# Performance work log

Hardware: AMD Instinct MI355X
Metric: run time of the kernel (lower is better)

## Reference

```python
import jax, jax.numpy as jnp
import numpy as np

N_NODES = 100000
N_EDGES = 1600000
NFEAT, NHID, NCLASS = 128, 64, 40


def setup_inputs() -> dict:
    key = jax.random.key(0)
    k = jax.random.split(key, 6)
    x = jax.random.normal(k[0], (N_NODES, NFEAT), dtype=jnp.float32)
    edge_index = jax.random.randint(k[1], (2, N_EDGES), 0, N_NODES, dtype=jnp.int64)
    edge_weight = jax.random.uniform(k[2], (N_EDGES,), dtype=jnp.float32)
    # Glorot-style init as in PyG GCNConv.reset_parameters
    W1 = jax.random.normal(k[3], (NFEAT, NHID), dtype=jnp.float32) * (1.0 / np.sqrt(NFEAT))
    b1 = jnp.zeros((NHID,), dtype=jnp.float32)
    W2 = jax.random.normal(k[4], (NHID, NCLASS), dtype=jnp.float32) * (1.0 / np.sqrt(NHID))
    b2 = jnp.zeros((NCLASS,), dtype=jnp.float32)
    return {"x": x, "edge_index": edge_index, "edge_weight": edge_weight,
            "W1": W1, "b1": b1, "W2": W2, "b2": b2}


def _gcn_conv(x, edge_index, edge_weight, W, b):
    """PyG GCNConv: add self-loops, symmetric gcn_norm, linear, scatter-add, bias."""
    n = x.shape[0]
    loop = jnp.arange(n)
    row = jnp.concatenate([edge_index[0], loop])  # source nodes
    col = jnp.concatenate([edge_index[1], loop])  # target nodes
    w = jnp.concatenate([edge_weight, jnp.ones((n,), edge_weight.dtype)])
    deg = jax.ops.segment_sum(w, col, num_segments=n)          # [N]
    dinv = jnp.where(deg > 0, jax.lax.rsqrt(deg), 0.0)
    norm = dinv[row] * w * dinv[col]                           # [E+N]
    h = x @ W                                                  # [N, out]
    msg = norm[:, None] * h[row]                               # gather: [E+N, out]
    out = jax.ops.segment_sum(msg, col, num_segments=n)        # scatter-add: [N, out]
    return out + b


def reference(x, edge_index, edge_weight, W1, b1, W2, b2):
    h = jax.nn.relu(_gcn_conv(x, edge_index, edge_weight, W1, b1))
    # F.dropout with training=False is identity (eval mode)
    return _gcn_conv(h, edge_index, edge_weight, W2, b2)
```

## Files before the change

kernel.cpp:

```cpp
#include <hip/hip_runtime.h>
#include <hip/hip_bf16.h>

#define N_NODES 100000
#define N_EDGES 1600000
#define NFEAT 128
#define NHID 64
#define NCLASS 40
#define CAP 64

#define BIN_SHIFT 9
#define BIN_NODES 512
#define NBIN ((N_NODES + BIN_NODES - 1) / BIN_NODES)
#define SCAP 10240
#define CHUNK 2048
#define LCAP 16

using frag_ab = __attribute__((ext_vector_type(8))) short;
using frag_cd = __attribute__((ext_vector_type(4))) float;


__device__ __forceinline__ unsigned pack2(float a, float b) {
    unsigned ua = __float_as_uint(a), ub = __float_as_uint(b);
    unsigned ra = (ua + 0x7FFFu + ((ua >> 16) & 1u)) >> 16;
    unsigned rb = (ub + 0x7FFFu + ((ub >> 16) & 1u)) >> 16;
    return ra | (rb << 16);
}
__device__ __forceinline__ unsigned short bf16rtn(float f) {
    unsigned u = __float_as_uint(f);
    return (unsigned short)((u + 0x7FFFu + ((u >> 16) & 1u)) >> 16);
}
__device__ __forceinline__ float lo16(unsigned w) { return __uint_as_float(w << 16); }
__device__ __forceinline__ float hi16(unsigned w) { return __uint_as_float(w & 0xFFFF0000u); }


__global__ __launch_bounds__(256) void bin_kernel(const int* __restrict__ ei,
                                                  const float* __restrict__ ew,
                                                  int* __restrict__ bincnt,
                                                  uint2* __restrict__ staging) {
    __shared__ int lcnt[NBIN];
    __shared__ int gbase[NBIN];
    __shared__ int scanbuf[256];
    __shared__ int totals;
    __shared__ uint2 lbuf[NBIN * LCAP];
    int t = threadIdx.x;
    for (int i = t; i < NBIN; i += 256) lcnt[i] = 0;
    __syncthreads();

    int base = blockIdx.x * CHUNK;
#pragma unroll
    for (int u = 0; u < CHUNK / 256; ++u) {
        int e = base + u * 256 + t;
        if (e < N_EDGES) {
            int c = ei[N_EDGES + e];
            int r = ei[e];
            float w = ew[e];
            unsigned wq = (unsigned)fminf(w * 32768.0f, 32767.0f);
            uint2 en = make_uint2(((unsigned)r << 15) | wq, (unsigned)c);
            int b = c >> BIN_SHIFT;
            int p = atomicAdd(&lcnt[b], 1);
            if (p < LCAP) {
                lbuf[b * LCAP + p] = en;
            } else {
                int g = atomicAdd(&bincnt[b], 1);
                if (g < SCAP) staging[(size_t)b * SCAP + g] = en;
            }
        }
    }
    __syncthreads();

    int clamped = (t < NBIN) ? min(lcnt[t], LCAP) : 0;
    if (t < NBIN) gbase[t] = (clamped > 0) ? atomicAdd(&bincnt[t], clamped) : 0;
    scanbuf[t] = clamped;
    __syncthreads();
    for (int o = 1; o < 256; o <<= 1) {
        int add = (t >= o) ? scanbuf[t - o] : 0;
        __syncthreads();
        scanbuf[t] += add;
        __syncthreads();
    }
    if (t < NBIN) lcnt[t] = scanbuf[t] - clamped;
    if (t == NBIN - 1) totals = scanbuf[t];
    __syncthreads();

    int total = totals;
    for (int i = t; i < total; i += 256) {
        int lo = 0, hi = NBIN - 1;
#pragma unroll
        for (int s = 0; s < 8; ++s) {
            int mid = (lo + hi + 1) >> 1;
            if (lcnt[mid] <= i) lo = mid; else hi = mid - 1;
        }
        int idx = i - lcnt[lo];
        int gp = gbase[lo] + idx;
        if (gp < SCAP) staging[(size_t)lo * SCAP + gp] = lbuf[lo * LCAP + idx];
    }
}


__global__ __launch_bounds__(256) void place_kernel(const int* __restrict__ bincnt,
                                                    const uint2* __restrict__ staging,
                                                    unsigned* __restrict__ bucket,
                                                    int* __restrict__ cnt,
                                                    float* __restrict__ dinv) {
    __shared__ int lpos[BIN_NODES];
    __shared__ float lws[BIN_NODES];
    int b = blockIdx.x;
    int t = threadIdx.x;
    for (int i = t; i < BIN_NODES; i += 256) { lpos[i] = 0; lws[i] = 0.0f; }
    __syncthreads();

    int nodebase = b << BIN_SHIFT;
    int n = bincnt[b];
    if (n > SCAP) n = SCAP;
    const uint2* st = staging + (size_t)b * SCAP;
    for (int i = t; i < n; i += 256) {
        uint2 en = st[i];
        int local = (int)en.y - nodebase;
        int p = atomicAdd(&lpos[local], 1);
        if (p < CAP) bucket[((size_t)en.y << 6) + p] = en.x;
        atomicAdd(&lws[local], (float)(en.x & 32767u) * (1.0f / 32768.0f));
    }
    __syncthreads();
    for (int i = t; i < BIN_NODES; i += 256) {
        int node = nodebase + i;
        if (node < N_NODES) {
            cnt[node] = min(lpos[i], CAP);
            dinv[node] = rsqrtf(1.0f + lws[i]);
        }
    }
}


__global__ __launch_bounds__(256) void w1prep_kernel(const float* __restrict__ W1,
                                                     unsigned short* __restrict__ w1t) {
    int idx = blockIdx.x * 256 + threadIdx.x;
    if (idx < NFEAT * NHID) {
        int k = idx >> 6, n = idx & 63;
        w1t[n * NFEAT + k] = bf16rtn(W1[idx]);
    }
}


__global__ __launch_bounds__(256) void gemm1_kernel(const float* __restrict__ x,
                                                    const unsigned short* __restrict__ w1t,
                                                    unsigned short* __restrict__ h1b) {
    __shared__ unsigned short sm[16384];
    int t = threadIdx.x;
    int row0 = blockIdx.x * 64;

#pragma unroll
    for (int p = 0; p < 4; ++p) {
        int id = p * 256 + t;
        int r = id >> 4;
        int c = id & 15;
        int gr = row0 + r; if (gr > N_NODES - 1) gr = N_NODES - 1;
        const float* src = x + (size_t)gr * NFEAT + c * 8;
        float4 f0 = *(const float4*)src;
        float4 f1 = *(const float4*)(src + 4);
        uint4 pk = make_uint4(pack2(f0.x, f0.y), pack2(f0.z, f0.w),
                              pack2(f1.x, f1.y), pack2(f1.z, f1.w));
        int cs = c ^ (r & 15);
        *(uint4*)(&sm[r * 128 + cs * 8]) = pk;
    }
    const uint4* wt4 = (const uint4*)w1t;
#pragma unroll
    for (int p = 0; p < 4; ++p) {
        int id = p * 256 + t;
        int n = id >> 4;
        int c = id & 15;
        uint4 v = wt4[id];
        int cs = c ^ (n & 15);
        *(uint4*)(&sm[8192 + n * 128 + cs * 8]) = v;
    }
    __syncthreads();

    int w = t >> 6, l = t & 63;
    int li = l & 15, q = l >> 4;
    int arow = w * 16 + li;

    frag_cd acc0 = {0.f, 0.f, 0.f, 0.f};
    frag_cd acc1 = {0.f, 0.f, 0.f, 0.f};
    frag_cd acc2 = {0.f, 0.f, 0.f, 0.f};
    frag_cd acc3 = {0.f, 0.f, 0.f, 0.f};

#pragma unroll
    for (int kc = 0; kc < 4; ++kc) {
        int cc = (kc * 4 + q) ^ li;
        frag_ab a  = *(const frag_ab*)(&sm[arow * 128 + cc * 8]);
        frag_ab b0 = *(const frag_ab*)(&sm[8192 + (0 * 16 + li) * 128 + cc * 8]);
        frag_ab b1 = *(const frag_ab*)(&sm[8192 + (1 * 16 + li) * 128 + cc * 8]);
        frag_ab b2 = *(const frag_ab*)(&sm[8192 + (2 * 16 + li) * 128 + cc * 8]);
        frag_ab b3 = *(const frag_ab*)(&sm[8192 + (3 * 16 + li) * 128 + cc * 8]);
        acc0 = __builtin_amdgcn_mfma_f32_16x16x32_bf16(a, b0, acc0, 0, 0, 0);
        acc1 = __builtin_amdgcn_mfma_f32_16x16x32_bf16(a, b1, acc1, 0, 0, 0);
        acc2 = __builtin_amdgcn_mfma_f32_16x16x32_bf16(a, b2, acc2, 0, 0, 0);
        acc3 = __builtin_amdgcn_mfma_f32_16x16x32_bf16(a, b3, acc3, 0, 0, 0);
    }

#pragma unroll
    for (int reg = 0; reg < 4; ++reg) {
        int rrow = row0 + w * 16 + q * 4 + reg;
        if (rrow < N_NODES) {
            unsigned short* dst = h1b + (size_t)rrow * NHID + li;
            dst[0]  = bf16rtn(acc0[reg]);
            dst[16] = bf16rtn(acc1[reg]);
            dst[32] = bf16rtn(acc2[reg]);
            dst[48] = bf16rtn(acc3[reg]);
        }
    }
}


__global__ __launch_bounds__(256) void gather1_kernel(
        const int* __restrict__ cnt, const unsigned* __restrict__ bucket,
        const float* __restrict__ dinv, const unsigned short* __restrict__ h1b,
        const float* __restrict__ b1, float* __restrict__ relu1) {
    int t = threadIdx.x;
    int lane = t & 63;
    int wave = t >> 6;
    int g = lane >> 3;
    int l = lane & 7;
    int node = (blockIdx.x * 4 + wave) * 8 + g;
    bool nvalid = node < N_NODES;
    int nd = nvalid ? node : N_NODES - 1;
    int d = cnt[nd];
    float dc = dinv[nd];

    uint4 eb0 = *(const uint4*)(bucket + ((size_t)nd << 6) + l * 8);
    uint4 eb1 = *(const uint4*)(bucket + ((size_t)nd << 6) + l * 8 + 4);
    int rl[8]; float wl[8];
#pragma unroll
    for (int k = 0; k < 8; ++k) {
        unsigned e = (k < 4) ? ((const unsigned*)&eb0)[k] : ((const unsigned*)&eb1)[k - 4];
        int slot = l * 8 + k;
        bool ok = slot < d;
        int r = ok ? (int)(e >> 15) : 0;
        rl[k] = r;
        wl[k] = ok ? (float)(e & 32767u) * (1.0f / 32768.0f) * dinv[r] : 0.0f;
    }

    uint4 hs = *(const uint4*)(h1b + (size_t)nd * NHID + l * 8);
    float acc[8];
#pragma unroll
    for (int k = 0; k < 4; ++k) {
        unsigned w = ((const unsigned*)&hs)[k];
        acc[2 * k] = dc * lo16(w);
        acc[2 * k + 1] = dc * hi16(w);
    }

    for (int j = 0; j < d; j += 8) {
        int src = (g << 3) + (j >> 3);
        int r[8]; float w[8];
#pragma unroll
        for (int k = 0; k < 8; ++k) { r[k] = __shfl(rl[k], src); w[k] = __shfl(wl[k], src); }
        uint4 v[8];
#pragma unroll
        for (int k = 0; k < 8; ++k)
            v[k] = *(const uint4*)(h1b + (size_t)r[k] * NHID + l * 8);
#pragma unroll
        for (int k = 0; k < 8; ++k) {
#pragma unroll
            for (int q = 0; q < 4; ++q) {
                unsigned ww = ((const unsigned*)&v[k])[q];
                acc[2 * q] += w[k] * lo16(ww);
                acc[2 * q + 1] += w[k] * hi16(ww);
            }
        }
    }
    if (nvalid) {
        float4 bv0 = *(const float4*)(b1 + l * 8);
        float4 bv1 = *(const float4*)(b1 + l * 8 + 4);
        float4 o0 = make_float4(fmaxf(dc * acc[0] + bv0.x, 0.0f), fmaxf(dc * acc[1] + bv0.y, 0.0f),
                                fmaxf(dc * acc[2] + bv0.z, 0.0f), fmaxf(dc * acc[3] + bv0.w, 0.0f));
        float4 o1 = make_float4(fmaxf(dc * acc[4] + bv1.x, 0.0f), fmaxf(dc * acc[5] + bv1.y, 0.0f),
                                fmaxf(dc * acc[6] + bv1.z, 0.0f), fmaxf(dc * acc[7] + bv1.w, 0.0f));
        *(float4*)(relu1 + (size_t)node * NHID + l * 8) = o0;
        *(float4*)(relu1 + (size_t)node * NHID + l * 8 + 4) = o1;
    }
}


__global__ __launch_bounds__(256) void gemm2_kernel(const float* __restrict__ in,
                                                    const float* __restrict__ W2,
                                                    unsigned short* __restrict__ h2b) {
    __shared__ float sB[NHID * NCLASS];
    int t = threadIdx.x;
    for (int i = t; i < NHID * NCLASS; i += 256) sB[i] = W2[i];
    __syncthreads();

    int row = blockIdx.x * 256 + t;
    bool valid = row < N_NODES;
    int r = valid ? row : N_NODES - 1;
    float acc[NCLASS] = {};

#pragma unroll 2
    for (int k = 0; k < NHID; k += 4) {
        float4 a = *(const float4*)(in + (size_t)r * NHID + k);
#pragma unroll
        for (int kk = 0; kk < 4; ++kk) {
            float av = (kk == 0) ? a.x : (kk == 1) ? a.y : (kk == 2) ? a.z : a.w;
#pragma unroll
            for (int cg = 0; cg < 10; ++cg) {
                float4 bb = *(const float4*)(sB + (k + kk) * NCLASS + cg * 4);
                acc[cg * 4 + 0] += av * bb.x;
                acc[cg * 4 + 1] += av * bb.y;
                acc[cg * 4 + 2] += av * bb.z;
                acc[cg * 4 + 3] += av * bb.w;
            }
        }
    }
    if (valid) {
#pragma unroll
        for (int cg = 0; cg < 5; ++cg) {
            uint4 p;
            p.x = pack2(acc[cg * 8 + 0], acc[cg * 8 + 1]);
            p.y = pack2(acc[cg * 8 + 2], acc[cg * 8 + 3]);
            p.z = pack2(acc[cg * 8 + 4], acc[cg * 8 + 5]);
            p.w = pack2(acc[cg * 8 + 6], acc[cg * 8 + 7]);
            *(uint4*)(h2b + (size_t)row * NCLASS + cg * 8) = p;
        }
    }
}


__global__ __launch_bounds__(256) void gather2_kernel(
        const int* __restrict__ cnt, const unsigned* __restrict__ bucket,
        const float* __restrict__ dinv, const unsigned short* __restrict__ h2b,
        const float* __restrict__ b2, float* __restrict__ out) {
    int t = threadIdx.x;
    int lane = t & 63;
    int wave = t >> 6;
    int g = lane >> 4;
    int l = lane & 15;
    int node = (blockIdx.x * 4 + wave) * 4 + g;
    bool nvalid = node < N_NODES;
    int nd = nvalid ? node : N_NODES - 1;
    int d = cnt[nd];
    float dc = dinv[nd];
    bool fvalid = (l < 10);

    uint4 eb = *(const uint4*)(bucket + ((size_t)nd << 6) + l * 4);
    int rl[4]; float wl[4];
#pragma unroll
    for (int k = 0; k < 4; ++k) {
        unsigned e = ((const unsigned*)&eb)[k];
        int slot = l * 4 + k;
        bool ok = slot < d;
        int r = ok ? (int)(e >> 15) : 0;
        rl[k] = r;
        wl[k] = ok ? (float)(e & 32767u) * (1.0f / 32768.0f) * dinv[r] : 0.0f;
    }

    float acc[4] = {};
    int lc = fvalid ? l * 4 : 0;
    if (fvalid) {
        uint2 hs = *(const uint2*)(h2b + (size_t)nd * NCLASS + lc);
        acc[0] = dc * lo16(hs.x); acc[1] = dc * hi16(hs.x);
        acc[2] = dc * lo16(hs.y); acc[3] = dc * hi16(hs.y);
    }

    for (int j = 0; j < d; j += 4) {
        int src = (g << 4) + (j >> 2);
        int r0 = __shfl(rl[0], src), r1 = __shfl(rl[1], src);
        int r2 = __shfl(rl[2], src), r3 = __shfl(rl[3], src);
        float w0 = __shfl(wl[0], src), w1 = __shfl(wl[1], src);
        float w2 = __shfl(wl[2], src), w3 = __shfl(wl[3], src);
        if (fvalid) {
            uint2 v0 = *(const uint2*)(h2b + (size_t)r0 * NCLASS + lc);
            uint2 v1 = *(const uint2*)(h2b + (size_t)r1 * NCLASS + lc);
            uint2 v2 = *(const uint2*)(h2b + (size_t)r2 * NCLASS + lc);
            uint2 v3 = *(const uint2*)(h2b + (size_t)r3 * NCLASS + lc);
            acc[0] += w0 * lo16(v0.x) + w1 * lo16(v1.x) + w2 * lo16(v2.x) + w3 * lo16(v3.x);
            acc[1] += w0 * hi16(v0.x) + w1 * hi16(v1.x) + w2 * hi16(v2.x) + w3 * hi16(v3.x);
            acc[2] += w0 * lo16(v0.y) + w1 * lo16(v1.y) + w2 * lo16(v2.y) + w3 * lo16(v3.y);
            acc[3] += w0 * hi16(v0.y) + w1 * hi16(v1.y) + w2 * hi16(v2.y) + w3 * hi16(v3.y);
        }
    }
    if (nvalid && fvalid) {
        float4 bv = *(const float4*)(b2 + l * 4);
        *(float4*)(out + (size_t)node * NCLASS + l * 4) =
            make_float4(dc * acc[0] + bv.x, dc * acc[1] + bv.y,
                        dc * acc[2] + bv.z, dc * acc[3] + bv.w);
    }
}


extern "C" void kernel_launch(void* const* d_in, const int* in_sizes, int n_in,
                              void* d_out, int out_size, void* d_ws, size_t ws_size,
                              hipStream_t stream) {
    const float* x  = (const float*)d_in[0];
    const int*   ei = (const int*)d_in[1];
    const float* ew = (const float*)d_in[2];
    const float* W1 = (const float*)d_in[3];
    const float* b1 = (const float*)d_in[4];
    const float* W2 = (const float*)d_in[5];
    const float* b2 = (const float*)d_in[6];
    float* out = (float*)d_out;

    int*            bincnt = (int*)d_ws;
    int*            cnt    = bincnt + 256;
    float*          dinv   = (float*)(cnt + 100352);
    unsigned*       bucket = (unsigned*)(dinv + 100352);
    unsigned short* h1b    = (unsigned short*)(bucket + (size_t)N_NODES * CAP);
    float*          relu1  = (float*)(h1b + (size_t)N_NODES * NHID);
    unsigned short* w1t    = (unsigned short*)(relu1 + (size_t)N_NODES * NHID);
    uint2*          staging = (uint2*)relu1;
    unsigned short* h2b    = h1b;

    hipMemsetAsync(bincnt, 0, NBIN * sizeof(int), stream);

    w1prep_kernel<<<32, 256, 0, stream>>>(W1, w1t);
    bin_kernel<<<(N_EDGES + CHUNK - 1) / CHUNK, 256, 0, stream>>>(ei, ew, bincnt, staging);
    place_kernel<<<NBIN, 256, 0, stream>>>(bincnt, staging, bucket, cnt, dinv);

    gemm1_kernel<<<(N_NODES + 63) / 64, 256, 0, stream>>>(x, w1t, h1b);
    gather1_kernel<<<(N_NODES + 31) / 32, 256, 0, stream>>>(cnt, bucket, dinv, h1b, b1, relu1);

    gemm2_kernel<<<(N_NODES + 255) / 256, 256, 0, stream>>>(relu1, W2, h2b);
    gather2_kernel<<<(N_NODES + 15) / 16, 256, 0, stream>>>(cnt, bucket, dinv, h2b, b2, out);
}
```

Baseline: 275.4 us.

## Use MFMA bf16 for second GEMM, store relu1 as bf16, simplify binning

The second GEMM now runs on bf16 MFMA 16x16x32 instructions. Its operands are staged in swizzled LDS tiles, and W2 is pre-transposed to bf16 in a merged prep kernel. The first aggregation writes its ReLU output as bf16 instead of fp32, which halves that intermediate traffic. Edge binning switches from a local-buffer-plus-scan scheme to a two-pass count/reserve/scatter with smaller chunks, and place_kernel uses 512 threads. The risks are extra bf16 rounding on the hidden activations and one more workgroup barrier pass in binning.

```diff
diff --git a/kernel.cpp b/kernel.cpp
--- a/kernel.cpp
+++ b/kernel.cpp
@@ -12,8 +12,7 @@
 #define BIN_NODES 512
 #define NBIN ((N_NODES + BIN_NODES - 1) / BIN_NODES)
 #define SCAP 10240
-#define CHUNK 2048
-#define LCAP 16
+#define CHUNK 1024
 
 using frag_ab = __attribute__((ext_vector_type(8))) short;
 using frag_cd = __attribute__((ext_vector_type(4))) float;
@@ -39,65 +38,49 @@
                                                   uint2* __restrict__ staging) {
     __shared__ int lcnt[NBIN];
     __shared__ int gbase[NBIN];
-    __shared__ int scanbuf[256];
-    __shared__ int totals;
-    __shared__ uint2 lbuf[NBIN * LCAP];
     int t = threadIdx.x;
     for (int i = t; i < NBIN; i += 256) lcnt[i] = 0;
     __syncthreads();
 
     int base = blockIdx.x * CHUNK;
-#pragma unroll
-    for (int u = 0; u < CHUNK / 256; ++u) {
+    int c[4]; int rr[4]; float w[4];
+#pragma unroll
+    for (int u = 0; u < 4; ++u) {
         int e = base + u * 256 + t;
         if (e < N_EDGES) {
-            int c = ei[N_EDGES + e];
-            int r = ei[e];
-            float w = ew[e];
-            unsigned wq = (unsigned)fminf(w * 32768.0f, 32767.0f);
-            uint2 en = make_uint2(((unsigned)r << 15) | wq, (unsigned)c);
-            int b = c >> BIN_SHIFT;
-            int p = atomicAdd(&lcnt[b], 1);
-            if (p < LCAP) {
-                lbuf[b * LCAP + p] = en;
-            } else {
-                int g = atomicAdd(&bincnt[b], 1);
-                if (g < SCAP) staging[(size_t)b * SCAP + g] = en;
-            }
-        }
-    }
-    __syncthreads();
-
-    int clamped = (t < NBIN) ? min(lcnt[t], LCAP) : 0;
-    if (t < NBIN) gbase[t] = (clamped > 0) ? atomicAdd(&bincnt[t], clamped) : 0;
-    scanbuf[t] = clamped;
-    __syncthreads();
-    for (int o = 1; o < 256; o <<= 1) {
-        int add = (t >= o) ? scanbuf[t - o] : 0;
-        __syncthreads();
-        scanbuf[t] += add;
-        __syncthreads();
-    }
-    if (t < NBIN) lcnt[t] = scanbuf[t] - clamped;
-    if (t == NBIN - 1) totals = scanbuf[t];
-    __syncthreads();
-
-    int total = totals;
-    for (int i = t; i < total; i += 256) {
-        int lo = 0, hi = NBIN - 1;
-#pragma unroll
-        for (int s = 0; s < 8; ++s) {
-            int mid = (lo + hi + 1) >> 1;
-            if (lcnt[mid] <= i) lo = mid; else hi = mid - 1;
-        }
-        int idx = i - lcnt[lo];
-        int gp = gbase[lo] + idx;
-        if (gp < SCAP) staging[(size_t)lo * SCAP + gp] = lbuf[lo * LCAP + idx];
-    }
-}
-
-
-__global__ __launch_bounds__(256) void place_kernel(const int* __restrict__ bincnt,
+            c[u] = ei[N_EDGES + e];
+            rr[u] = ei[e];
+            w[u] = ew[e];
+        } else {
+            c[u] = -1;
+        }
+    }
+#pragma unroll
+    for (int u = 0; u < 4; ++u)
+        if (c[u] >= 0) atomicAdd(&lcnt[c[u] >> BIN_SHIFT], 1);
+    __syncthreads();
+    if (t < NBIN) {
+        int n = lcnt[t];
+        gbase[t] = (n > 0) ? atomicAdd(&bincnt[t], n) : 0;
+    }
+    __syncthreads();
+    if (t < NBIN) lcnt[t] = 0;
+    __syncthreads();
+#pragma unroll
+    for (int u = 0; u < 4; ++u) {
+        if (c[u] >= 0) {
+            int b = c[u] >> BIN_SHIFT;
+            unsigned wq = (unsigned)fminf(w[u] * 32768.0f, 32767.0f);
+            int p = gbase[b] + atomicAdd(&lcnt[b], 1);
+            if (p < SCAP)
+                staging[(size_t)b * SCAP + p] =
+                    make_uint2(((unsigned)rr[u] << 15) | wq, (unsigned)c[u]);
+        }
+    }
+}
+
+
+__global__ __launch_bounds__(512) void place_kernel(const int* __restrict__ bincnt,
                                                     const uint2* __restrict__ staging,
                                                     unsigned* __restrict__ bucket,
                                                     int* __restrict__ cnt,
@@ -106,14 +89,14 @@
     __shared__ float lws[BIN_NODES];
     int b = blockIdx.x;
     int t = threadIdx.x;
-    for (int i = t; i < BIN_NODES; i += 256) { lpos[i] = 0; lws[i] = 0.0f; }
+    for (int i = t; i < BIN_NODES; i += 512) { lpos[i] = 0; lws[i] = 0.0f; }
     __syncthreads();
 
     int nodebase = b << BIN_SHIFT;
     int n = bincnt[b];
     if (n > SCAP) n = SCAP;
     const uint2* st = staging + (size_t)b * SCAP;
-    for (int i = t; i < n; i += 256) {
+    for (int i = t; i < n; i += 512) {
         uint2 en = st[i];
         int local = (int)en.y - nodebase;
         int p = atomicAdd(&lpos[local], 1);
@@ -121,7 +104,7 @@
         atomicAdd(&lws[local], (float)(en.x & 32767u) * (1.0f / 32768.0f));
     }
     __syncthreads();
-    for (int i = t; i < BIN_NODES; i += 256) {
+    for (int i = t; i < BIN_NODES; i += 512) {
         int node = nodebase + i;
         if (node < N_NODES) {
             cnt[node] = min(lpos[i], CAP);
@@ -131,12 +114,19 @@
 }
 
 
-__global__ __launch_bounds__(256) void w1prep_kernel(const float* __restrict__ W1,
-                                                     unsigned short* __restrict__ w1t) {
+__global__ __launch_bounds__(256) void prep_kernel(const float* __restrict__ W1,
+                                                   const float* __restrict__ W2,
+                                                   unsigned short* __restrict__ w1t,
+                                                   unsigned short* __restrict__ w2t) {
     int idx = blockIdx.x * 256 + threadIdx.x;
     if (idx < NFEAT * NHID) {
         int k = idx >> 6, n = idx & 63;
         w1t[n * NFEAT + k] = bf16rtn(W1[idx]);
+    }
+    int idx2 = idx - NFEAT * NHID;
+    if (idx2 >= 0 && idx2 < NHID * NCLASS) {
+        int k = idx2 / NCLASS, n = idx2 - k * NCLASS;
+        w2t[n * NHID + k] = bf16rtn(W2[idx2]);
     }
 }
 
@@ -214,7 +204,7 @@
 __global__ __launch_bounds__(256) void gather1_kernel(
         const int* __restrict__ cnt, const unsigned* __restrict__ bucket,
         const float* __restrict__ dinv, const unsigned short* __restrict__ h1b,
-        const float* __restrict__ b1, float* __restrict__ relu1) {
+        const float* __restrict__ b1, unsigned short* __restrict__ relu1b) {
     int t = threadIdx.x;
     int lane = t & 63;
     int wave = t >> 6;
@@ -270,54 +260,70 @@
     if (nvalid) {
         float4 bv0 = *(const float4*)(b1 + l * 8);
         float4 bv1 = *(const float4*)(b1 + l * 8 + 4);
-        float4 o0 = make_float4(fmaxf(dc * acc[0] + bv0.x, 0.0f), fmaxf(dc * acc[1] + bv0.y, 0.0f),
-                                fmaxf(dc * acc[2] + bv0.z, 0.0f), fmaxf(dc * acc[3] + bv0.w, 0.0f));
-        float4 o1 = make_float4(fmaxf(dc * acc[4] + bv1.x, 0.0f), fmaxf(dc * acc[5] + bv1.y, 0.0f),
-                                fmaxf(dc * acc[6] + bv1.z, 0.0f), fmaxf(dc * acc[7] + bv1.w, 0.0f));
-        *(float4*)(relu1 + (size_t)node * NHID + l * 8) = o0;
-        *(float4*)(relu1 + (size_t)node * NHID + l * 8 + 4) = o1;
-    }
-}
-
-
-__global__ __launch_bounds__(256) void gemm2_kernel(const float* __restrict__ in,
-                                                    const float* __restrict__ W2,
+        float o0 = fmaxf(dc * acc[0] + bv0.x, 0.0f), o1 = fmaxf(dc * acc[1] + bv0.y, 0.0f);
+        float o2 = fmaxf(dc * acc[2] + bv0.z, 0.0f), o3 = fmaxf(dc * acc[3] + bv0.w, 0.0f);
+        float o4 = fmaxf(dc * acc[4] + bv1.x, 0.0f), o5 = fmaxf(dc * acc[5] + bv1.y, 0.0f);
+        float o6 = fmaxf(dc * acc[6] + bv1.z, 0.0f), o7 = fmaxf(dc * acc[7] + bv1.w, 0.0f);
+        uint4 pk = make_uint4(pack2(o0, o1), pack2(o2, o3), pack2(o4, o5), pack2(o6, o7));
+        *(uint4*)(relu1b + (size_t)node * NHID + l * 8) = pk;
+    }
+}
+
+
+__global__ __launch_bounds__(256) void gemm2_kernel(const unsigned short* __restrict__ relu1b,
+                                                    const unsigned short* __restrict__ w2t,
                                                     unsigned short* __restrict__ h2b) {
-    __shared__ float sB[NHID * NCLASS];
-    int t = threadIdx.x;
-    for (int i = t; i < NHID * NCLASS; i += 256) sB[i] = W2[i];
-    __syncthreads();
-
-    int row = blockIdx.x * 256 + t;
-    bool valid = row < N_NODES;
-    int r = valid ? row : N_NODES - 1;
-    float acc[NCLASS] = {};
-
-#pragma unroll 2
-    for (int k = 0; k < NHID; k += 4) {
-        float4 a = *(const float4*)(in + (size_t)r * NHID + k);
-#pragma unroll
-        for (int kk = 0; kk < 4; ++kk) {
-            float av = (kk == 0) ? a.x : (kk == 1) ? a.y : (kk == 2) ? a.z : a.w;
-#pragma unroll
-            for (int cg = 0; cg < 10; ++cg) {
-                float4 bb = *(const float4*)(sB + (k + kk) * NCLASS + cg * 4);
-                acc[cg * 4 + 0] += av * bb.x;
-                acc[cg * 4 + 1] += av * bb.y;
-                acc[cg * 4 + 2] += av * bb.z;
-                acc[cg * 4 + 3] += av * bb.w;
-            }
-        }
-    }
-    if (valid) {
-#pragma unroll
-        for (int cg = 0; cg < 5; ++cg) {
-            uint4 p;
-            p.x = pack2(acc[cg * 8 + 0], acc[cg * 8 + 1]);
-            p.y = pack2(acc[cg * 8 + 2], acc[cg * 8 + 3]);
-            p.z = pack2(acc[cg * 8 + 4], acc[cg * 8 + 5]);
-            p.w = pack2(acc[cg * 8 + 6], acc[cg * 8 + 7]);
-            *(uint4*)(h2b + (size_t)row * NCLASS + cg * 8) = p;
+    __shared__ unsigned short sa[64 * 64];
+    __shared__ unsigned short sb[48 * 64];
+    int t = threadIdx.x;
+    int row0 = blockIdx.x * 64;
+
+#pragma unroll
+    for (int p = 0; p < 2; ++p) {
+        int id = p * 256 + t;
+        int r = id >> 3, cj = id & 7;
+        int gr = row0 + r; if (gr > N_NODES - 1) gr = N_NODES - 1;
+        uint4 v = *(const uint4*)(relu1b + (size_t)gr * NHID + cj * 8);
+        int cs = cj ^ (r & 7);
+        *(uint4*)(&sa[r * 64 + cs * 8]) = v;
+    }
+    for (int id = t; id < 384; id += 256) {
+        int n = id >> 3, cj = id & 7;
+        uint4 v = make_uint4(0u, 0u, 0u, 0u);
+        if (n < NCLASS) v = *(const uint4*)(w2t + n * NHID + cj * 8);
+        int cs = cj ^ (n & 7);
+        *(uint4*)(&sb[n * 64 + cs * 8]) = v;
+    }
+    __syncthreads();
+
+    int w = t >> 6, l = t & 63;
+    int li = l & 15, q = l >> 4;
+    int arow = w * 16 + li;
+
+    frag_cd acc0 = {0.f, 0.f, 0.f, 0.f};
+    frag_cd acc1 = {0.f, 0.f, 0.f, 0.f};
+    frag_cd acc2 = {0.f, 0.f, 0.f, 0.f};
+
+#pragma unroll
+    for (int kc = 0; kc < 2; ++kc) {
+        int cc = (kc * 4 + q) ^ (li & 7);
+        frag_ab a  = *(const frag_ab*)(&sa[arow * 64 + cc * 8]);
+        frag_ab b0 = *(const frag_ab*)(&sb[(0 + li) * 64 + cc * 8]);
+        frag_ab b1 = *(const frag_ab*)(&sb[(16 + li) * 64 + cc * 8]);
+        frag_ab b2 = *(const frag_ab*)(&sb[(32 + li) * 64 + cc * 8]);
+        acc0 = __builtin_amdgcn_mfma_f32_16x16x32_bf16(a, b0, acc0, 0, 0, 0);
+        acc1 = __builtin_amdgcn_mfma_f32_16x16x32_bf16(a, b1, acc1, 0, 0, 0);
+        acc2 = __builtin_amdgcn_mfma_f32_16x16x32_bf16(a, b2, acc2, 0, 0, 0);
+    }
+
+#pragma unroll
+    for (int reg = 0; reg < 4; ++reg) {
+        int rrow = row0 + w * 16 + q * 4 + reg;
+        if (rrow < N_NODES) {
+            unsigned short* dst = h2b + (size_t)rrow * NCLASS;
+            dst[li] = bf16rtn(acc0[reg]);
+            dst[16 + li] = bf16rtn(acc1[reg]);
+            if (li < 8) dst[32 + li] = bf16rtn(acc2[reg]);
         }
     }
 }
@@ -397,25 +403,27 @@
     const float* b2 = (const float*)d_in[6];
     float* out = (float*)d_out;
 
-    int*            bincnt = (int*)d_ws;
-    int*            cnt    = bincnt + 256;
-    float*          dinv   = (float*)(cnt + 100352);
-    unsigned*       bucket = (unsigned*)(dinv + 100352);
-    unsigned short* h1b    = (unsigned short*)(bucket + (size_t)N_NODES * CAP);
-    float*          relu1  = (float*)(h1b + (size_t)N_NODES * NHID);
-    unsigned short* w1t    = (unsigned short*)(relu1 + (size_t)N_NODES * NHID);
-    uint2*          staging = (uint2*)relu1;
-    unsigned short* h2b    = h1b;
+    int*            bincnt  = (int*)d_ws;
+    int*            cnt     = bincnt + 256;
+    float*          dinv    = (float*)(cnt + 100352);
+    unsigned*       bucket  = (unsigned*)(dinv + 100352);
+    unsigned short* h1b     = (unsigned short*)(bucket + (size_t)N_NODES * CAP);
+    unsigned short* region2 = h1b + (size_t)N_NODES * NHID;
+    uint2*          staging = (uint2*)region2;
+    unsigned short* relu1b  = region2;
+    unsigned short* w1t     = region2 + (size_t)NBIN * SCAP * 4;
+    unsigned short* w2t     = w1t + NFEAT * NHID;
+    unsigned short* h2b     = h1b;
 
     hipMemsetAsync(bincnt, 0, NBIN * sizeof(int), stream);
 
-    w1prep_kernel<<<32, 256, 0, stream>>>(W1, w1t);
+    prep_kernel<<<42, 256, 0, stream>>>(W1, W2, w1t, w2t);
     bin_kernel<<<(N_EDGES + CHUNK - 1) / CHUNK, 256, 0, stream>>>(ei, ew, bincnt, staging);
-    place_kernel<<<NBIN, 256, 0, stream>>>(bincnt, staging, bucket, cnt, dinv);
+    place_kernel<<<NBIN, 512, 0, stream>>>(bincnt, staging, bucket, cnt, dinv);
 
     gemm1_kernel<<<(N_NODES + 63) / 64, 256, 0, stream>>>(x, w1t, h1b);
-    gather1_kernel<<<(N_NODES + 31) / 32, 256, 0, stream>>>(cnt, bucket, dinv, h1b, b1, relu1);
-
-    gemm2_kernel<<<(N_NODES + 255) / 256, 256, 0, stream>>>(relu1, W2, h2b);
+    gather1_kernel<<<(N_NODES + 31) / 32, 256, 0, stream>>>(cnt, bucket, dinv, h1b, b1, relu1b);
+
+    gemm2_kernel<<<(N_NODES + 63) / 64, 256, 0, stream>>>(relu1b, w2t, h2b);
     gather2_kernel<<<(N_NODES + 15) / 16, 256, 0, stream>>>(cnt, bucket, dinv, h2b, b2, out);
 }
```

New measurement: 257.6 us. -6.4%, faster.
